# Performance work log

Hardware: AMD Instinct MI355X
Metric: run time of the kernel (lower is better)

## Reference

```python
import jax, jax.numpy as jnp
import numpy as np

NUM_EXPERTS = 8
HIDDEN = 2048
EXPERT_DIM = 2048  # intermediate_size per shard (tp_size=1)
TOTAL_TOKENS = 32768  # divisible by NUM_EXPERTS


def setup_inputs() -> dict:
    key = jax.random.key(0)
    k1, k2, k3 = jax.random.split(key, 3)
    hidden_states = jax.random.normal(k1, (TOTAL_TOKENS, HIDDEN), dtype=jnp.float32)
    # (E, H, 2*D): gate and up projections concatenated on last dim
    gate_up_proj = jax.random.normal(k2, (NUM_EXPERTS, HIDDEN, 2 * EXPERT_DIM), dtype=jnp.float32) * 0.02
    # (E, D, H)
    down_proj = jax.random.normal(k3, (NUM_EXPERTS, EXPERT_DIM, HIDDEN), dtype=jnp.float32) * 0.02
    return {"hidden_states": hidden_states, "gate_up_proj": gate_up_proj, "down_proj": down_proj}


def reference(hidden_states, gate_up_proj, down_proj):
    E, H = gate_up_proj.shape[0], gate_up_proj.shape[1]
    # tokens are pre-sorted per expert: (E, T, H)
    x = hidden_states.reshape(E, -1, H)
    # grouped GEMM: (E,T,H) @ (E,H,2D) -> (E,T,2D)
    gate_up = jnp.einsum('eth,ehd->etd', x, gate_up_proj)
    gate, up = jnp.split(gate_up, 2, axis=-1)
    # SwiGLU epilogue then down projection: (E,T,D) @ (E,D,H) -> (E,T,H)
    act = up * jax.nn.silu(gate)
    out = jnp.einsum('etd,edh->eth', act, down_proj)
    # tp_size=1 -> all_reduce is identity
    return out.reshape(-1, H)
```

## Files before the change

kernel.cpp:

```cpp
#include <hip/hip_runtime.h>


#define E_EXPERTS 8
#define TPE 4096
#define KD 2048

typedef __bf16 bf16_t;
typedef __bf16 bf16x4 __attribute__((ext_vector_type(4)));
typedef __bf16 bf16x8 __attribute__((ext_vector_type(8)));
typedef float f32x4 __attribute__((ext_vector_type(4)));

#define GLOAD16(src, dst)                                               \
  __builtin_amdgcn_global_load_lds(                                     \
      (const __attribute__((address_space(1))) void*)(src),             \
      (__attribute__((address_space(3))) void*)(dst), 16, 0, 0)

__global__ void cvt_f32_bf16_kernel(const float* __restrict__ in,
                                    bf16_t* __restrict__ out, long n4) {
  long i = (long)blockIdx.x * blockDim.x + threadIdx.x;
  const long stride = (long)gridDim.x * blockDim.x;
  const float4* in4 = (const float4*)in;
  bf16x4* out4 = (bf16x4*)out;
  for (; i < n4; i += stride) {
    float4 v = in4[i];
    bf16x4 o = {(bf16_t)v.x, (bf16_t)v.y, (bf16_t)v.z, (bf16_t)v.w};
    out4[i] = o;
  }
}

__global__ void transpose_cvt_kernel(const float* __restrict__ W,
                                     bf16_t* __restrict__ WT, int K, int N) {
  __shared__ float tile[64][65];
  const int e = blockIdx.z;
  const float* Wp = W + (size_t)e * K * N;
  bf16_t* Tp = WT + (size_t)e * N * K;
  const int n0 = blockIdx.x * 64, k0 = blockIdx.y * 64;
  const int rr = threadIdx.x >> 4;
  const int cc = (threadIdx.x & 15) * 4;
#pragma unroll
  for (int p = 0; p < 4; ++p) {
    const int k = rr + p * 16;
    float4 v = *(const float4*)(Wp + (size_t)(k0 + k) * N + n0 + cc);
    tile[k][cc + 0] = v.x;
    tile[k][cc + 1] = v.y;
    tile[k][cc + 2] = v.z;
    tile[k][cc + 3] = v.w;
  }
  __syncthreads();
#pragma unroll
  for (int p = 0; p < 4; ++p) {
    const int n = rr + p * 16;
    bf16x4 o;
#pragma unroll
    for (int j = 0; j < 4; ++j) o[j] = (bf16_t)tile[cc + j][n];
    *(bf16x4*)(Tp + (size_t)(n0 + n) * K + k0 + cc) = o;
  }
}

template <bool FUSED, int NTN>
__global__ __launch_bounds__(512, 4) void moe_gemm_tlp_kernel(
    const bf16_t* __restrict__ A, const bf16_t* __restrict__ Bm,
    void* __restrict__ Cout) {
  constexpr int NT = KD / 32;

  __shared__ alignas(16) bf16_t As[3][64][64];
  __shared__ alignas(16) bf16_t Bs[3][128][64];

  const int NWG = gridDim.x;
  int wg = blockIdx.x;
  wg = (wg & 7) * (NWG >> 3) + (wg >> 3);
  const int e = wg / (32 * NTN);
  const int rem = wg % (32 * NTN);
  const int mt = rem / NTN, ntile = rem % NTN;
  const int t0 = mt * 128, n0 = ntile * 256;

  const int tid = threadIdx.x;
  const int wid = tid >> 6, lane = tid & 63;
  const int wr = wid >> 2, wc = wid & 3;

  const bf16_t* Ae = A + (size_t)e * TPE * KD + (size_t)t0 * KD;
  const bf16_t* Be = Bm + (size_t)e * (size_t)(FUSED ? 4096 : 2048) * KD;

  const int sp = lane >> 3;
  const int lc = lane & 7;

  const int pAr = wid * 8 + sp;
  const int cAr = lc ^ (pAr & 7);
  const bf16_t* aSrc = Ae + (size_t)(pAr + 64 * (cAr >> 2)) * KD + (cAr & 3) * 8;

  const bf16_t* bSrc[2];
#pragma unroll
  for (int i = 0; i < 2; ++i) {
    const int p = wid * 16 + i * 8 + sp;
    const int c = lc ^ (p & 7);
    const int R = n0 + p + 128 * (c >> 2);
    int srow;
    if constexpr (FUSED)
      srow = ((R >> 5) << 4) + (R & 15) + ((R >> 4) & 1) * 2048;
    else
      srow = R;
    bSrc[i] = Be + (size_t)srow * KD + (c & 3) * 8;
  }

  auto stageA = [&](int kt, int slot) {
    const int k0 = (kt & (NT - 1)) * 32;
    GLOAD16(aSrc + k0, &As[slot][wid * 8][0]);
  };
  auto stageB = [&](int kt, int slot) {
    const int k0 = (kt & (NT - 1)) * 32;
#pragma unroll
    for (int i = 0; i < 2; ++i)
      GLOAD16(bSrc[i] + k0, &Bs[slot][wid * 16 + i * 8][0]);
  };

  const int la = lane & 15, kg4 = lane >> 4;

  const bf16_t* pA[4];
#pragma unroll
  for (int m = 0; m < 4; ++m) {
    const int r = wr * 64 + m * 16 + la;
    const int p = r & 63, h = r >> 6;
    const int c = (h * 4 + kg4) ^ (p & 7);
    pA[m] = &As[0][p][c * 8];
  }
  const bf16_t* pB[4];
#pragma unroll
  for (int q = 0; q < 2; ++q)
#pragma unroll
    for (int jf = 0; jf < 2; ++jf) {
      const int R = wc * 64 + q * 32 + jf * 16 + la;
      const int p = R & 127, h = R >> 7;
      const int c = (h * 4 + kg4) ^ (p & 7);
      pB[q * 2 + jf] = &Bs[0][p][c * 8];
    }

  f32x4 acc[4][4] = {};
  bf16x8 am[4];
  bf16x8 bn0, bn1, bn2, bn3;

#define W2 asm volatile("s_waitcnt lgkmcnt(2)" ::: "memory")
#define W0 asm volatile("s_waitcnt lgkmcnt(0)" ::: "memory")
#define VMC3 asm volatile("s_waitcnt vmcnt(3)" ::: "memory")
#define BAR __builtin_amdgcn_s_barrier()
#define SCHED0 __builtin_amdgcn_sched_barrier(0)
#define PRIO1 __builtin_amdgcn_s_setprio(1)
#define PRIO0 __builtin_amdgcn_s_setprio(0)

#define TILE(t, S, S2)                                                       \
  do {                                                                       \
    am[0] = *(const bf16x8*)(pA[0] + (S) * 4096);                            \
    am[1] = *(const bf16x8*)(pA[1] + (S) * 4096);                            \
    am[2] = *(const bf16x8*)(pA[2] + (S) * 4096);                            \
    am[3] = *(const bf16x8*)(pA[3] + (S) * 4096);                            \
    bn0 = *(const bf16x8*)(pB[0] + (S) * 8192);                              \
    bn1 = *(const bf16x8*)(pB[1] + (S) * 8192);                              \
    bn2 = *(const bf16x8*)(pB[2] + (S) * 8192);                              \
    bn3 = *(const bf16x8*)(pB[3] + (S) * 8192);                              \
    stageA((t) + 2, S2);                                                     \
    stageB((t) + 2, S2);                                                     \
    W2; SCHED0;                                                              \
    PRIO1;                                                                   \
    _Pragma("unroll") for (int m = 0; m < 4; ++m) {                          \
      acc[m][0] = __builtin_amdgcn_mfma_f32_16x16x32_bf16(am[m], bn0,        \
                                                          acc[m][0], 0, 0, 0); \
      acc[m][1] = __builtin_amdgcn_mfma_f32_16x16x32_bf16(am[m], bn1,        \
                                                          acc[m][1], 0, 0, 0); \
    }                                                                        \
    PRIO0;                                                                   \
    W0; SCHED0;                                                              \
    PRIO1;                                                                   \
    _Pragma("unroll") for (int m = 0; m < 4; ++m) {                          \
      acc[m][2] = __builtin_amdgcn_mfma_f32_16x16x32_bf16(am[m], bn2,        \
                                                          acc[m][2], 0, 0, 0); \
      acc[m][3] = __builtin_amdgcn_mfma_f32_16x16x32_bf16(am[m], bn3,        \
                                                          acc[m][3], 0, 0, 0); \
    }                                                                        \
    PRIO0;                                                                   \
    VMC3;                                                                    \
    BAR; SCHED0;                                                             \
  } while (0)

  stageA(0, 0); stageB(0, 0);
  stageA(1, 1); stageB(1, 1);
  VMC3;
  BAR; SCHED0;

  int t = 0;
  for (; t < NT - 3; t += 3) {
    TILE(t, 0, 2);
    TILE(t + 1, 1, 0);
    TILE(t + 2, 2, 1);
  }
  TILE(t, 0, 2);

  const int rbase = t0 + wr * 64;
  if constexpr (FUSED) {
    bf16_t* Cp = (bf16_t*)Cout + (size_t)e * TPE * KD;
    const int jb = (n0 >> 1) + 32 * wc;
#pragma unroll
    for (int m = 0; m < 4; ++m)
#pragma unroll
      for (int q = 0; q < 2; ++q)
#pragma unroll
        for (int r = 0; r < 4; ++r) {
          const int row = rbase + m * 16 + kg4 * 4 + r;
          const int col = jb + q * 16 + la;
          const float g = acc[m][2 * q][r], u = acc[m][2 * q + 1][r];
          const float sg = 1.0f / (1.0f + __expf(-g));
          Cp[(size_t)row * KD + col] = (bf16_t)(u * g * sg);
        }
  } else {
    float* Cp = (float*)Cout + (size_t)e * TPE * KD;
#pragma unroll
    for (int m = 0; m < 4; ++m)
#pragma unroll
      for (int n = 0; n < 4; ++n)
#pragma unroll
        for (int r = 0; r < 4; ++r) {
          const int row = rbase + m * 16 + kg4 * 4 + r;
          const int col = n0 + wc * 64 + n * 16 + la;
          Cp[(size_t)row * KD + col] = acc[m][n][r];
        }
  }
#undef W2
#undef W0
#undef VMC3
#undef BAR
#undef SCHED0
#undef PRIO1
#undef PRIO0
#undef TILE
}

extern "C" void kernel_launch(void* const* d_in, const int* in_sizes, int n_in,
                              void* d_out, int out_size, void* d_ws,
                              size_t ws_size, hipStream_t stream) {
  const float* hs = (const float*)d_in[0];
  const float* w1 = (const float*)d_in[1];
  const float* w2 = (const float*)d_in[2];

  char* ws = (char*)d_ws;
  bf16_t* xb = (bf16_t*)(ws);
  bf16_t* w1t = (bf16_t*)(ws + (size_t)134217728);
  bf16_t* w2t = (bf16_t*)(ws + (size_t)268435456);
  bf16_t* act = (bf16_t*)(ws + (size_t)335544320);

  const long n4 = (long)E_EXPERTS * TPE * KD / 4;
  transpose_cvt_kernel<<<dim3(32, 32, 8), 256, 0, stream>>>(w2, w2t, 2048, 2048);
  cvt_f32_bf16_kernel<<<2048, 256, 0, stream>>>(hs, xb, n4);
  transpose_cvt_kernel<<<dim3(64, 32, 8), 256, 0, stream>>>(w1, w1t, 2048, 4096);
  moe_gemm_tlp_kernel<true, 16><<<4096, 512, 0, stream>>>(xb, w1t, (void*)act);
  moe_gemm_tlp_kernel<false, 8><<<2048, 512, 0, stream>>>(act, w2t, d_out);
}
```

Before: 1.095 ms.

## Load GEMM A operand directly into registers, bypassing LDS staging

Removes the LDS staging buffer for the activation (A) tile and instead has each wave load its A fragments directly from global memory into registers, double-buffered with a one-step prefetch. B remains staged in LDS via a 3-slot ring, now indexed by runtime slot counters with a non-unrolled loop, and B fragments are loaded in two halves to save registers. This cuts LDS capacity and ds_read traffic but makes each A element be fetched from global/L2 by four waves instead of once, and adds vector-memory wait dependencies in the inner loop.

```diff
diff --git a/kernel.cpp b/kernel.cpp
--- a/kernel.cpp
+++ b/kernel.cpp
@@ -58,12 +58,11 @@
 }
 
 template <bool FUSED, int NTN>
-__global__ __launch_bounds__(512, 4) void moe_gemm_tlp_kernel(
+__global__ __launch_bounds__(512, 4) void moe_gemm_areg_kernel(
     const bf16_t* __restrict__ A, const bf16_t* __restrict__ Bm,
     void* __restrict__ Cout) {
   constexpr int NT = KD / 32;
 
-  __shared__ alignas(16) bf16_t As[3][64][64];
   __shared__ alignas(16) bf16_t Bs[3][128][64];
 
   const int NWG = gridDim.x;
@@ -83,10 +82,6 @@
 
   const int sp = lane >> 3;
   const int lc = lane & 7;
-
-  const int pAr = wid * 8 + sp;
-  const int cAr = lc ^ (pAr & 7);
-  const bf16_t* aSrc = Ae + (size_t)(pAr + 64 * (cAr >> 2)) * KD + (cAr & 3) * 8;
 
   const bf16_t* bSrc[2];
 #pragma unroll
@@ -102,10 +97,6 @@
     bSrc[i] = Be + (size_t)srow * KD + (c & 3) * 8;
   }
 
-  auto stageA = [&](int kt, int slot) {
-    const int k0 = (kt & (NT - 1)) * 32;
-    GLOAD16(aSrc + k0, &As[slot][wid * 8][0]);
-  };
   auto stageB = [&](int kt, int slot) {
     const int k0 = (kt & (NT - 1)) * 32;
 #pragma unroll
@@ -114,15 +105,16 @@
   };
 
   const int la = lane & 15, kg4 = lane >> 4;
-
-  const bf16_t* pA[4];
-#pragma unroll
-  for (int m = 0; m < 4; ++m) {
-    const int r = wr * 64 + m * 16 + la;
-    const int p = r & 63, h = r >> 6;
-    const int c = (h * 4 + kg4) ^ (p & 7);
-    pA[m] = &As[0][p][c * 8];
-  }
+  const bf16_t* aG = Ae + (size_t)(wr * 64 + la) * KD + kg4 * 8;
+
+  auto apref = [&](int kt, bf16x8 (&dst)[4]) {
+    const int k0 = (kt & (NT - 1)) * 32;
+    const bf16_t* p = aG + k0;
+#pragma unroll
+    for (int m = 0; m < 4; ++m)
+      dst[m] = *(const bf16x8*)(p + (size_t)m * 16 * KD);
+  };
+
   const bf16_t* pB[4];
 #pragma unroll
   for (int q = 0; q < 2; ++q)
@@ -135,63 +127,60 @@
     }
 
   f32x4 acc[4][4] = {};
-  bf16x8 am[4];
-  bf16x8 bn0, bn1, bn2, bn3;
-
-#define W2 asm volatile("s_waitcnt lgkmcnt(2)" ::: "memory")
+  bf16x8 aP[4], aQ[4];
+  bf16x8 bn[2];
+
 #define W0 asm volatile("s_waitcnt lgkmcnt(0)" ::: "memory")
-#define VMC3 asm volatile("s_waitcnt vmcnt(3)" ::: "memory")
+#define VMC6 asm volatile("s_waitcnt vmcnt(6)" ::: "memory")
 #define BAR __builtin_amdgcn_s_barrier()
 #define SCHED0 __builtin_amdgcn_sched_barrier(0)
 #define PRIO1 __builtin_amdgcn_s_setprio(1)
 #define PRIO0 __builtin_amdgcn_s_setprio(0)
 
-#define TILE(t, S, S2)                                                       \
+#define TILE(t, AU, AV)                                                      \
   do {                                                                       \
-    am[0] = *(const bf16x8*)(pA[0] + (S) * 4096);                            \
-    am[1] = *(const bf16x8*)(pA[1] + (S) * 4096);                            \
-    am[2] = *(const bf16x8*)(pA[2] + (S) * 4096);                            \
-    am[3] = *(const bf16x8*)(pA[3] + (S) * 4096);                            \
-    bn0 = *(const bf16x8*)(pB[0] + (S) * 8192);                              \
-    bn1 = *(const bf16x8*)(pB[1] + (S) * 8192);                              \
-    bn2 = *(const bf16x8*)(pB[2] + (S) * 8192);                              \
-    bn3 = *(const bf16x8*)(pB[3] + (S) * 8192);                              \
-    stageA((t) + 2, S2);                                                     \
-    stageB((t) + 2, S2);                                                     \
-    W2; SCHED0;                                                              \
+    bn[0] = *(const bf16x8*)(pB[0] + s * 8192);                              \
+    bn[1] = *(const bf16x8*)(pB[1] + s * 8192);                              \
+    stageB((t) + 2, s2);                                                     \
+    apref((t) + 1, AV);                                                      \
+    W0; SCHED0;                                                              \
+    VMC6; SCHED0;                                                            \
     PRIO1;                                                                   \
     _Pragma("unroll") for (int m = 0; m < 4; ++m) {                          \
-      acc[m][0] = __builtin_amdgcn_mfma_f32_16x16x32_bf16(am[m], bn0,        \
+      acc[m][0] = __builtin_amdgcn_mfma_f32_16x16x32_bf16(AU[m], bn[0],      \
                                                           acc[m][0], 0, 0, 0); \
-      acc[m][1] = __builtin_amdgcn_mfma_f32_16x16x32_bf16(am[m], bn1,        \
+      acc[m][1] = __builtin_amdgcn_mfma_f32_16x16x32_bf16(AU[m], bn[1],      \
                                                           acc[m][1], 0, 0, 0); \
     }                                                                        \
     PRIO0;                                                                   \
+    bn[0] = *(const bf16x8*)(pB[2] + s * 8192);                              \
+    bn[1] = *(const bf16x8*)(pB[3] + s * 8192);                              \
     W0; SCHED0;                                                              \
     PRIO1;                                                                   \
     _Pragma("unroll") for (int m = 0; m < 4; ++m) {                          \
-      acc[m][2] = __builtin_amdgcn_mfma_f32_16x16x32_bf16(am[m], bn2,        \
+      acc[m][2] = __builtin_amdgcn_mfma_f32_16x16x32_bf16(AU[m], bn[0],      \
                                                           acc[m][2], 0, 0, 0); \
-      acc[m][3] = __builtin_amdgcn_mfma_f32_16x16x32_bf16(am[m], bn3,        \
+      acc[m][3] = __builtin_amdgcn_mfma_f32_16x16x32_bf16(AU[m], bn[1],      \
                                                           acc[m][3], 0, 0, 0); \
     }                                                                        \
     PRIO0;                                                                   \
-    VMC3;                                                                    \
     BAR; SCHED0;                                                             \
+    s = (s == 2) ? 0 : s + 1;                                                \
+    s2 = (s2 == 2) ? 0 : s2 + 1;                                             \
   } while (0)
 
-  stageA(0, 0); stageB(0, 0);
-  stageA(1, 1); stageB(1, 1);
-  VMC3;
+  stageB(0, 0);
+  stageB(1, 1);
+  apref(0, aP);
+  VMC6;
   BAR; SCHED0;
 
-  int t = 0;
-  for (; t < NT - 3; t += 3) {
-    TILE(t, 0, 2);
-    TILE(t + 1, 1, 0);
-    TILE(t + 2, 2, 1);
-  }
-  TILE(t, 0, 2);
+  int s = 0, s2 = 2;
+#pragma unroll 1
+  for (int t = 0; t < NT; t += 2) {
+    TILE(t, aP, aQ);
+    TILE(t + 1, aQ, aP);
+  }
 
   const int rbase = t0 + wr * 64;
   if constexpr (FUSED) {
@@ -222,9 +211,8 @@
           Cp[(size_t)row * KD + col] = acc[m][n][r];
         }
   }
-#undef W2
 #undef W0
-#undef VMC3
+#undef VMC6
 #undef BAR
 #undef SCHED0
 #undef PRIO1
@@ -249,6 +237,6 @@
   transpose_cvt_kernel<<<dim3(32, 32, 8), 256, 0, stream>>>(w2, w2t, 2048, 2048);
   cvt_f32_bf16_kernel<<<2048, 256, 0, stream>>>(hs, xb, n4);
   transpose_cvt_kernel<<<dim3(64, 32, 8), 256, 0, stream>>>(w1, w1t, 2048, 4096);
-  moe_gemm_tlp_kernel<true, 16><<<4096, 512, 0, stream>>>(xb, w1t, (void*)act);
-  moe_gemm_tlp_kernel<false, 8><<<2048, 512, 0, stream>>>(act, w2t, d_out);
-}
+  moe_gemm_areg_kernel<true, 16><<<4096, 512, 0, stream>>>(xb, w1t, (void*)act);
+  moe_gemm_areg_kernel<false, 8><<<2048, 512, 0, stream>>>(act, w2t, d_out);
+}
```

After: 1.891 ms. +72.7%, slower.
